# Kernel tuning notes

Measured on AMD Instinct MI355X. Metric: run time of the kernel, lower is better.

Reference implementation:

```python
import jax, jax.numpy as jnp
import numpy as np

NUM_HEADS = 8
HIDDEN_DIM = 256
QUERY_DIM = 256
HEAD_DIM = HIDDEN_DIM // NUM_HEADS
NORM_FACT = float(HIDDEN_DIM / NUM_HEADS) ** (-0.5)


def setup_inputs() -> dict:
    key = jax.random.key(0)
    k1, k2, k3, k4, k5 = jax.random.split(key, 5)
    B, Q, H, W = 16, 100, 64, 64
    q = jax.random.normal(k1, (B, Q, QUERY_DIM), dtype=jnp.float32)
    k = jax.random.normal(k2, (B, QUERY_DIM, H, W), dtype=jnp.float32)
    mask = jax.random.randint(k3, (B, H, W), 0, 2).astype(jnp.bool_)
    # xavier_uniform for [hidden, query] linear weights
    limit = float(np.sqrt(6.0 / (HIDDEN_DIM + QUERY_DIM)))
    Wq = jax.random.uniform(k4, (HIDDEN_DIM, QUERY_DIM), minval=-limit, maxval=limit, dtype=jnp.float32)
    Wk = jax.random.uniform(k5, (HIDDEN_DIM, QUERY_DIM), minval=-limit, maxval=limit, dtype=jnp.float32)
    bq = jnp.zeros((HIDDEN_DIM,), dtype=jnp.float32)
    bk = jnp.zeros((HIDDEN_DIM,), dtype=jnp.float32)
    return {"q": q, "k": k, "Wq": Wq, "bq": bq, "Wk": Wk, "bk": bk, "mask": mask}


def reference(q, k, Wq, bq, Wk, bk, mask):
    B, Q, _ = q.shape
    _, C, H, W = k.shape
    # q projection: [B, Q, hidden]
    qp = jnp.einsum('bqc,hc->bqh', q, Wq) + bq
    # k projection via 1x1 conv == channelwise linear: [B, hidden, H, W]
    kp = jnp.einsum('bchw,oc->bohw', k, Wk) + bk[None, :, None, None]
    # split heads: qh [B,Q,nh,hd], kh [B,nh,hd,H,W]
    qh = qp.reshape(B, Q, NUM_HEADS, HEAD_DIM)
    kh = kp.reshape(B, NUM_HEADS, HEAD_DIM, H, W)
    # scores [B,Q,nh,H,W]
    weights = jnp.einsum('bqnd,bndhw->bqnhw', qh, kh) * NORM_FACT
    # masked fill: mask [B,H,W] -> broadcast over (Q, heads)
    weights = jnp.where(mask[:, None, None, :, :], -jnp.inf, weights)
    # softmax jointly over (heads, H, W), as in torch flatten(2)
    flat = weights.reshape(B, Q, NUM_HEADS * H * W)
    flat = jax.nn.softmax(flat, axis=-1)
    return flat.reshape(B, Q, NUM_HEADS, H, W)
```

## Files before the change

### kernel.cpp

```cpp
#include <hip/hip_runtime.h>
#include <hip/hip_bf16.h>
#include <math.h>

#define BB 16
#define QQ 100
#define NH 8
#define HD 32
#define HWN 4096
#define NORM_FACT 0.17677669529663687f
#define QPAD 112

typedef short bf16x8_t __attribute__((ext_vector_type(8)));
typedef float f32x4_t  __attribute__((ext_vector_type(4)));

__device__ __forceinline__ unsigned short bf16bits(float f) {
    __hip_bfloat16 h = __float2bfloat16(f);
    return __builtin_bit_cast(unsigned short, h);
}
__device__ __forceinline__ float bf16tof(unsigned short u) {
    union { unsigned int i; float f; } x; x.i = (unsigned int)u << 16; return x.f;
}

__global__ void k_prep(const float* __restrict__ Wq, const float* __restrict__ Wk,
                       float* __restrict__ WqT, unsigned short* __restrict__ Wkbf) {
    int idx = blockIdx.x;
    int h = threadIdx.x;
    if (idx < 256) {
        WqT[idx * 256 + h] = Wq[h * 256 + idx];
    } else {
        int r = idx - 256;
        Wkbf[r * 256 + h] = bf16bits(Wk[r * 256 + h]);
    }
}

__global__ __launch_bounds__(256) void k_qproj(const float* __restrict__ q,
                                               const float* __restrict__ WqT,
                                               const float* __restrict__ bq,
                                               unsigned short* __restrict__ qphi,
                                               unsigned short* __restrict__ qplo) {
    int blk = blockIdx.x;
    int b = blk / 28, q0 = (blk % 28) * 4;
    int h = threadIdx.x;
    size_t obase = ((size_t)b * QPAD + q0) * 256 + h;
    if (q0 >= QQ) {
#pragma unroll
        for (int i = 0; i < 4; ++i) { qphi[obase + i * 256] = 0; qplo[obase + i * 256] = 0; }
        return;
    }
    __shared__ float qsh[4][256];
    int ibase = (b * QQ + q0) * 256;
#pragma unroll
    for (int i = 0; i < 4; ++i) qsh[i][h] = q[ibase + i * 256 + h];
    __syncthreads();
    float bias = bq[h];
    float a0 = bias, a1 = bias, a2 = bias, a3 = bias;
    for (int c = 0; c < 256; ++c) {
        float wv = WqT[c * 256 + h];
        a0 = fmaf(qsh[0][c], wv, a0);
        a1 = fmaf(qsh[1][c], wv, a1);
        a2 = fmaf(qsh[2][c], wv, a2);
        a3 = fmaf(qsh[3][c], wv, a3);
    }
    float a[4] = {a0 * NORM_FACT, a1 * NORM_FACT, a2 * NORM_FACT, a3 * NORM_FACT};
#pragma unroll
    for (int i = 0; i < 4; ++i) {
        unsigned short hi = bf16bits(a[i]);
        qphi[obase + i * 256] = hi;
        qplo[obase + i * 256] = bf16bits(a[i] - bf16tof(hi));
    }
}

__global__ __launch_bounds__(256) void k_tconv(const float* __restrict__ k,
                                               unsigned short* __restrict__ kT) {
    int b = blockIdx.z, c0 = blockIdx.y * 64, hw0 = blockIdx.x * 64;
    int t = threadIdx.x;
    __shared__ float lds[64][65];
    const float* src = k + ((size_t)b * 256 + c0) * HWN + hw0;
    int col = t & 63, r0 = t >> 6;
#pragma unroll
    for (int i = 0; i < 16; ++i) {
        int r = i * 4 + r0;
        lds[r][col] = src[(size_t)r * HWN + col];
    }
    __syncthreads();
    int hw = t >> 2, cc = (t & 3) * 16;
    unsigned short* dst = kT + ((size_t)b * HWN + hw0 + hw) * 256 + c0 + cc;
    uint4 v0, v1;
    unsigned int* w0 = (unsigned int*)&v0;
    unsigned int* w1 = (unsigned int*)&v1;
#pragma unroll
    for (int j = 0; j < 4; ++j) {
        w0[j] = (unsigned int)bf16bits(lds[cc + 2*j + 0][hw])
              | ((unsigned int)bf16bits(lds[cc + 2*j + 1][hw]) << 16);
        w1[j] = (unsigned int)bf16bits(lds[cc + 8 + 2*j + 0][hw])
              | ((unsigned int)bf16bits(lds[cc + 8 + 2*j + 1][hw]) << 16);
    }
    *(uint4*)(dst)     = v0;
    *(uint4*)(dst + 8) = v1;
}

__global__ __launch_bounds__(256) void k_kproj(const unsigned short* __restrict__ kT,
                                               const unsigned short* __restrict__ Wkbf,
                                               const float* __restrict__ bk,
                                               unsigned short* __restrict__ kpT) {
    int b = blockIdx.y;
    int hwblk = blockIdx.x * 32;
    int t = threadIdx.x;
    int w = t >> 6, lane = t & 63;
    int hwt = w & 1, oh = w >> 1;
    int n15 = lane & 15;
    int kg = lane >> 4;
    int hw = hwblk + hwt * 16 + n15;

    f32x4_t acc[8];
#pragma unroll
    for (int m = 0; m < 8; ++m) acc[m] = f32x4_t{0.f, 0.f, 0.f, 0.f};

    const unsigned short* kTrow = kT + ((size_t)b * HWN + hw) * 256 + kg * 8;
    const unsigned short* wbase = Wkbf + ((size_t)(oh * 128 + n15)) * 256 + kg * 8;

#pragma unroll 2
    for (int ks = 0; ks < 8; ++ks) {
        bf16x8_t bfrag = *reinterpret_cast<const bf16x8_t*>(kTrow + ks * 32);
#pragma unroll
        for (int m = 0; m < 8; ++m) {
            bf16x8_t afrag = *reinterpret_cast<const bf16x8_t*>(wbase + (size_t)m * 16 * 256 + ks * 32);
            acc[m] = __builtin_amdgcn_mfma_f32_16x16x32_bf16(afrag, bfrag, acc[m], 0, 0, 0);
        }
    }

    __shared__ unsigned short tile2[32 * 264];
    int hw_l = hwt * 16 + n15;
#pragma unroll
    for (int m = 0; m < 8; ++m) {
        ushort4 pk;
        unsigned short* pkp = (unsigned short*)&pk;
#pragma unroll
        for (int r = 0; r < 4; ++r) {
            int o = oh * 128 + m * 16 + kg * 4 + r;
            pkp[r] = bf16bits(acc[m][r] + bk[o]);
        }
        *(ushort4*)&tile2[hw_l * 264 + oh * 128 + m * 16 + kg * 4] = pk;
    }
    __syncthreads();
    int row = t >> 3, sub = t & 7;
    unsigned short* dst = kpT + ((size_t)b * HWN + hwblk + row) * 256 + sub * 32;
    const unsigned short* srcl = &tile2[row * 264 + sub * 32];
#pragma unroll
    for (int j = 0; j < 4; ++j)
        *(uint4*)(dst + j * 8) = *(const uint4*)(srcl + j * 8);
}

__global__ __launch_bounds__(256) void k_sums(const unsigned short* __restrict__ qphi,
                                              const unsigned short* __restrict__ qplo,
                                              const unsigned short* __restrict__ kpT,
                                              const int* __restrict__ mask,
                                              float* __restrict__ partial) {
    int b = blockIdx.y;
    int hwblk = blockIdx.x * 64;
    int t = threadIdx.x, w = t >> 6, lane = t & 63;
    int n15 = lane & 15, kg = lane >> 4;
    int hw = hwblk + w * 16 + n15;
    float mm = mask[b * HWN + hw] ? 0.0f : 1.0f;
    const unsigned short* brow  = kpT  + ((size_t)(b * HWN + hw)) * 256 + kg * 8;
    const unsigned short* ahi_b = qphi + ((size_t)(b * QPAD + n15)) * 256 + kg * 8;
    const unsigned short* alo_b = qplo + ((size_t)(b * QPAD + n15)) * 256 + kg * 8;
    float sums[7][4] = {};
#pragma unroll 1
    for (int n = 0; n < NH; ++n) {
        bf16x8_t ahi[7], alo[7];
#pragma unroll
        for (int mt = 0; mt < 7; ++mt) {
            ahi[mt] = *reinterpret_cast<const bf16x8_t*>(ahi_b + (size_t)(mt * 16) * 256 + n * 32);
            alo[mt] = *reinterpret_cast<const bf16x8_t*>(alo_b + (size_t)(mt * 16) * 256 + n * 32);
        }
        bf16x8_t bfr = *reinterpret_cast<const bf16x8_t*>(brow + n * 32);
#pragma unroll
        for (int mt = 0; mt < 7; ++mt) {
            f32x4_t a2 = {0.f, 0.f, 0.f, 0.f};
            a2 = __builtin_amdgcn_mfma_f32_16x16x32_bf16(ahi[mt], bfr, a2, 0, 0, 0);
            a2 = __builtin_amdgcn_mfma_f32_16x16x32_bf16(alo[mt], bfr, a2, 0, 0, 0);
#pragma unroll
            for (int r = 0; r < 4; ++r)
                sums[mt][r] += __expf(a2[r]) * mm;
        }
    }
#pragma unroll
    for (int mt = 0; mt < 7; ++mt)
#pragma unroll
        for (int r = 0; r < 4; ++r) {
            float v = sums[mt][r];
            v += __shfl_xor(v, 1, 64);
            v += __shfl_xor(v, 2, 64);
            v += __shfl_xor(v, 4, 64);
            v += __shfl_xor(v, 8, 64);
            if (n15 == 0) {
                int qrow = mt * 16 + kg * 4 + r;
                partial[((size_t)b * QPAD + qrow) * 256 + blockIdx.x * 4 + w] = v;
            }
        }
}

__global__ __launch_bounds__(256) void k_invsum(const float* __restrict__ partial,
                                                float* __restrict__ inv) {
    int blk = blockIdx.x;
    int b = blk / QQ, qq = blk % QQ;
    const float* p = partial + ((size_t)b * QPAD + qq) * 256;
    int t = threadIdx.x;
    float v = p[t];
#pragma unroll
    for (int off = 32; off; off >>= 1) v += __shfl_xor(v, off, 64);
    __shared__ float red[4];
    if ((t & 63) == 0) red[t >> 6] = v;
    __syncthreads();
    if (t == 0) inv[blk] = 1.0f / (red[0] + red[1] + red[2] + red[3]);
}

__global__ __launch_bounds__(256) void k_write(const unsigned short* __restrict__ qphi,
                                               const unsigned short* __restrict__ qplo,
                                               const unsigned short* __restrict__ kpT,
                                               const int* __restrict__ mask,
                                               const float* __restrict__ inv,
                                               float* __restrict__ out) {
    int hws = blockIdx.x, qt = blockIdx.y, b = blockIdx.z;
    int t = threadIdx.x, w = t >> 6, lane = t & 63;
    int n15 = lane & 15, kg = lane >> 4;
    int hw0 = hws * 256 + w * 64;
    float mm[4];
#pragma unroll
    for (int ht = 0; ht < 4; ++ht)
        mm[ht] = mask[b * HWN + hw0 + ht * 16 + n15] ? 0.0f : 1.0f;
    float invq[4];
#pragma unroll
    for (int r = 0; r < 4; ++r) {
        int qrow = qt * 16 + kg * 4 + r;
        invq[r] = (qrow < QQ) ? inv[b * QQ + qrow] : 0.0f;
    }
    const unsigned short* ahi_b = qphi + ((size_t)(b * QPAD + qt * 16 + n15)) * 256 + kg * 8;
    const unsigned short* alo_b = qplo + ((size_t)(b * QPAD + qt * 16 + n15)) * 256 + kg * 8;
    const unsigned short* brow  = kpT  + ((size_t)(b * HWN + hw0 + n15)) * 256 + kg * 8;
    __shared__ float lt[4][16][68];
#pragma unroll 1
    for (int n = 0; n < NH; ++n) {
        bf16x8_t bf[4];
#pragma unroll
        for (int ht = 0; ht < 4; ++ht)
            bf[ht] = *reinterpret_cast<const bf16x8_t*>(brow + (size_t)(ht * 16) * 256 + n * 32);
        bf16x8_t ahi = *reinterpret_cast<const bf16x8_t*>(ahi_b + n * 32);
        bf16x8_t alo = *reinterpret_cast<const bf16x8_t*>(alo_b + n * 32);
#pragma unroll
        for (int ht = 0; ht < 4; ++ht) {
            f32x4_t acc = {0.f, 0.f, 0.f, 0.f};
            acc = __builtin_amdgcn_mfma_f32_16x16x32_bf16(ahi, bf[ht], acc, 0, 0, 0);
            acc = __builtin_amdgcn_mfma_f32_16x16x32_bf16(alo, bf[ht], acc, 0, 0, 0);
#pragma unroll
            for (int r = 0; r < 4; ++r)
                lt[w][kg * 4 + r][ht * 16 + n15] = __expf(acc[r]) * mm[ht] * invq[r];
        }
#pragma unroll
        for (int j = 0; j < 4; ++j) {
            int rr = j * 4 + kg;
            int qrow = qt * 16 + rr;
            f32x4_t v4 = *(const f32x4_t*)&lt[w][rr][n15 * 4];
            if (qrow < QQ)
                __builtin_nontemporal_store(v4,
                    (f32x4_t*)(out + (((size_t)(b * QQ + qrow)) * NH + n) * HWN + hw0 + n15 * 4));
        }
    }
}

extern "C" void kernel_launch(void* const* d_in, const int* in_sizes, int n_in,
                              void* d_out, int out_size, void* d_ws, size_t ws_size,
                              hipStream_t stream) {
    const float* q    = (const float*)d_in[0];
    const float* k    = (const float*)d_in[1];
    const float* Wq   = (const float*)d_in[2];
    const float* bq   = (const float*)d_in[3];
    const float* Wk   = (const float*)d_in[4];
    const float* bk   = (const float*)d_in[5];
    const int*   mask = (const int*)d_in[6];
    float* out = (float*)d_out;

    char* base = (char*)d_ws;
    unsigned short* kT   = (unsigned short*)(base);
    unsigned short* kpT  = (unsigned short*)(base + 33554432);
    unsigned short* qphi = (unsigned short*)(base + 67108864);
    unsigned short* qplo = (unsigned short*)(base + 68026368);
    float*  WqT     = (float*)(base + 68943872);
    unsigned short* Wkbf = (unsigned short*)(base + 69206016);
    float*  partial = (float*)(base + 69337088);
    float*  inv     = (float*)(base + 71172096);
    if (ws_size < (size_t)71178496) return;

    k_prep  <<<dim3(512), dim3(256), 0, stream>>>(Wq, Wk, WqT, Wkbf);
    k_qproj <<<dim3(448), dim3(256), 0, stream>>>(q, WqT, bq, qphi, qplo);
    k_tconv <<<dim3(64, 4, 16), dim3(256), 0, stream>>>(k, kT);
    k_kproj <<<dim3(128, 16), dim3(256), 0, stream>>>(kT, Wkbf, bk, kpT);
    k_sums  <<<dim3(64, 16), dim3(256), 0, stream>>>(qphi, qplo, kpT, mask, partial);
    k_invsum<<<dim3(1600), dim3(256), 0, stream>>>(partial, inv);
    k_write <<<dim3(16, 7, 16), dim3(256), 0, stream>>>(qphi, qplo, kpT, mask, inv, out);
}
```

Before: 223.0 us.

## Fuse k transpose into projection and regrid sums and write kernels by head

Drops the separate transpose/convert kernel. k_kproj2 now loads fp32 k tiles into LDS and converts them to bf16 fragments inside the MFMA loop, which removes a 32MB intermediate round trip. k_sums now launches one block per head instead of looping over heads, so partial sums grow to 2048 slots per row and k_invsum must reduce more values. k_write is regridded by head and loops over query tiles, and it drops the LDS staging in favour of direct scalar nontemporal stores, which may give less coalesced writes.

```diff
diff --git a/kernel.cpp b/kernel.cpp
--- a/kernel.cpp
+++ b/kernel.cpp
@@ -5,10 +5,10 @@
 #define BB 16
 #define QQ 100
 #define NH 8
-#define HD 32
 #define HWN 4096
 #define NORM_FACT 0.17677669529663687f
 #define QPAD 112
+#define NSLOT 2048
 
 typedef short bf16x8_t __attribute__((ext_vector_type(8)));
 typedef float f32x4_t  __attribute__((ext_vector_type(4)));
@@ -70,67 +70,59 @@
     }
 }
 
-__global__ __launch_bounds__(256) void k_tconv(const float* __restrict__ k,
-                                               unsigned short* __restrict__ kT) {
-    int b = blockIdx.z, c0 = blockIdx.y * 64, hw0 = blockIdx.x * 64;
-    int t = threadIdx.x;
-    __shared__ float lds[64][65];
-    const float* src = k + ((size_t)b * 256 + c0) * HWN + hw0;
-    int col = t & 63, r0 = t >> 6;
-#pragma unroll
-    for (int i = 0; i < 16; ++i) {
-        int r = i * 4 + r0;
-        lds[r][col] = src[(size_t)r * HWN + col];
-    }
-    __syncthreads();
-    int hw = t >> 2, cc = (t & 3) * 16;
-    unsigned short* dst = kT + ((size_t)b * HWN + hw0 + hw) * 256 + c0 + cc;
-    uint4 v0, v1;
-    unsigned int* w0 = (unsigned int*)&v0;
-    unsigned int* w1 = (unsigned int*)&v1;
-#pragma unroll
-    for (int j = 0; j < 4; ++j) {
-        w0[j] = (unsigned int)bf16bits(lds[cc + 2*j + 0][hw])
-              | ((unsigned int)bf16bits(lds[cc + 2*j + 1][hw]) << 16);
-        w1[j] = (unsigned int)bf16bits(lds[cc + 8 + 2*j + 0][hw])
-              | ((unsigned int)bf16bits(lds[cc + 8 + 2*j + 1][hw]) << 16);
-    }
-    *(uint4*)(dst)     = v0;
-    *(uint4*)(dst + 8) = v1;
-}
-
-__global__ __launch_bounds__(256) void k_kproj(const unsigned short* __restrict__ kT,
-                                               const unsigned short* __restrict__ Wkbf,
-                                               const float* __restrict__ bk,
-                                               unsigned short* __restrict__ kpT) {
+__global__ __launch_bounds__(256) void k_kproj2(const float* __restrict__ k,
+                                                const unsigned short* __restrict__ Wkbf,
+                                                const float* __restrict__ bk,
+                                                unsigned short* __restrict__ kpT) {
     int b = blockIdx.y;
     int hwblk = blockIdx.x * 32;
     int t = threadIdx.x;
     int w = t >> 6, lane = t & 63;
     int hwt = w & 1, oh = w >> 1;
-    int n15 = lane & 15;
-    int kg = lane >> 4;
-    int hw = hwblk + hwt * 16 + n15;
+    int n15 = lane & 15, kg = lane >> 4;
+
+    __shared__ float lds_f[32][268];
+    {
+        const float* kb = k + (size_t)b * 256 * HWN + hwblk;
+        int c_l = t >> 3, l8 = t & 7;
+#pragma unroll
+        for (int it = 0; it < 8; ++it) {
+            int c = it * 32 + c_l;
+            float4 v = *(const float4*)(kb + (size_t)c * HWN + l8 * 4);
+            lds_f[l8 * 4 + 0][c] = v.x;
+            lds_f[l8 * 4 + 1][c] = v.y;
+            lds_f[l8 * 4 + 2][c] = v.z;
+            lds_f[l8 * 4 + 3][c] = v.w;
+        }
+    }
+    __syncthreads();
 
     f32x4_t acc[8];
 #pragma unroll
     for (int m = 0; m < 8; ++m) acc[m] = f32x4_t{0.f, 0.f, 0.f, 0.f};
 
-    const unsigned short* kTrow = kT + ((size_t)b * HWN + hw) * 256 + kg * 8;
     const unsigned short* wbase = Wkbf + ((size_t)(oh * 128 + n15)) * 256 + kg * 8;
-
-#pragma unroll 2
+    int hw_l = hwt * 16 + n15;
+
+#pragma unroll
     for (int ks = 0; ks < 8; ++ks) {
-        bf16x8_t bfrag = *reinterpret_cast<const bf16x8_t*>(kTrow + ks * 32);
+        f32x4_t f0 = *(const f32x4_t*)&lds_f[hw_l][ks * 32 + kg * 8];
+        f32x4_t f1 = *(const f32x4_t*)&lds_f[hw_l][ks * 32 + kg * 8 + 4];
+        bf16x8_t bfrag;
+#pragma unroll
+        for (int j = 0; j < 4; ++j) {
+            bfrag[j]     = (short)bf16bits(f0[j]);
+            bfrag[4 + j] = (short)bf16bits(f1[j]);
+        }
 #pragma unroll
         for (int m = 0; m < 8; ++m) {
             bf16x8_t afrag = *reinterpret_cast<const bf16x8_t*>(wbase + (size_t)m * 16 * 256 + ks * 32);
             acc[m] = __builtin_amdgcn_mfma_f32_16x16x32_bf16(afrag, bfrag, acc[m], 0, 0, 0);
         }
     }
-
-    __shared__ unsigned short tile2[32 * 264];
-    int hw_l = hwt * 16 + n15;
+    __syncthreads();
+
+    unsigned short* tile2 = (unsigned short*)lds_f;
 #pragma unroll
     for (int m = 0; m < 8; ++m) {
         ushort4 pk;
@@ -140,12 +132,12 @@
             int o = oh * 128 + m * 16 + kg * 4 + r;
             pkp[r] = bf16bits(acc[m][r] + bk[o]);
         }
-        *(ushort4*)&tile2[hw_l * 264 + oh * 128 + m * 16 + kg * 4] = pk;
+        *(ushort4*)&tile2[(size_t)hw_l * 264 + oh * 128 + m * 16 + kg * 4] = pk;
     }
     __syncthreads();
     int row = t >> 3, sub = t & 7;
     unsigned short* dst = kpT + ((size_t)b * HWN + hwblk + row) * 256 + sub * 32;
-    const unsigned short* srcl = &tile2[row * 264 + sub * 32];
+    const unsigned short* srcl = &tile2[(size_t)row * 264 + sub * 32];
 #pragma unroll
     for (int j = 0; j < 4; ++j)
         *(uint4*)(dst + j * 8) = *(const uint4*)(srcl + j * 8);
@@ -156,58 +148,46 @@
                                               const unsigned short* __restrict__ kpT,
                                               const int* __restrict__ mask,
                                               float* __restrict__ partial) {
-    int b = blockIdx.y;
-    int hwblk = blockIdx.x * 64;
+    int hwb = blockIdx.x, n = blockIdx.y, b = blockIdx.z;
     int t = threadIdx.x, w = t >> 6, lane = t & 63;
     int n15 = lane & 15, kg = lane >> 4;
-    int hw = hwblk + w * 16 + n15;
+    int hw = hwb * 64 + w * 16 + n15;
     float mm = mask[b * HWN + hw] ? 0.0f : 1.0f;
-    const unsigned short* brow  = kpT  + ((size_t)(b * HWN + hw)) * 256 + kg * 8;
-    const unsigned short* ahi_b = qphi + ((size_t)(b * QPAD + n15)) * 256 + kg * 8;
-    const unsigned short* alo_b = qplo + ((size_t)(b * QPAD + n15)) * 256 + kg * 8;
-    float sums[7][4] = {};
-#pragma unroll 1
-    for (int n = 0; n < NH; ++n) {
-        bf16x8_t ahi[7], alo[7];
-#pragma unroll
-        for (int mt = 0; mt < 7; ++mt) {
-            ahi[mt] = *reinterpret_cast<const bf16x8_t*>(ahi_b + (size_t)(mt * 16) * 256 + n * 32);
-            alo[mt] = *reinterpret_cast<const bf16x8_t*>(alo_b + (size_t)(mt * 16) * 256 + n * 32);
-        }
-        bf16x8_t bfr = *reinterpret_cast<const bf16x8_t*>(brow + n * 32);
-#pragma unroll
-        for (int mt = 0; mt < 7; ++mt) {
-            f32x4_t a2 = {0.f, 0.f, 0.f, 0.f};
-            a2 = __builtin_amdgcn_mfma_f32_16x16x32_bf16(ahi[mt], bfr, a2, 0, 0, 0);
-            a2 = __builtin_amdgcn_mfma_f32_16x16x32_bf16(alo[mt], bfr, a2, 0, 0, 0);
-#pragma unroll
-            for (int r = 0; r < 4; ++r)
-                sums[mt][r] += __expf(a2[r]) * mm;
-        }
-    }
-#pragma unroll
-    for (int mt = 0; mt < 7; ++mt)
+    bf16x8_t bfr = *reinterpret_cast<const bf16x8_t*>(
+        kpT + ((size_t)(b * HWN + hw)) * 256 + n * 32 + kg * 8);
+    const unsigned short* ahi_b = qphi + ((size_t)(b * QPAD + n15)) * 256 + n * 32 + kg * 8;
+    const unsigned short* alo_b = qplo + ((size_t)(b * QPAD + n15)) * 256 + n * 32 + kg * 8;
+    int slot = (hwb * 4 + w) * 8 + n;
+    float* pbase = partial + (size_t)b * QPAD * NSLOT + slot;
+#pragma unroll
+    for (int mt = 0; mt < 7; ++mt) {
+        bf16x8_t ahi = *reinterpret_cast<const bf16x8_t*>(ahi_b + (size_t)(mt * 16) * 256);
+        bf16x8_t alo = *reinterpret_cast<const bf16x8_t*>(alo_b + (size_t)(mt * 16) * 256);
+        f32x4_t a2 = {0.f, 0.f, 0.f, 0.f};
+        a2 = __builtin_amdgcn_mfma_f32_16x16x32_bf16(ahi, bfr, a2, 0, 0, 0);
+        a2 = __builtin_amdgcn_mfma_f32_16x16x32_bf16(alo, bfr, a2, 0, 0, 0);
 #pragma unroll
         for (int r = 0; r < 4; ++r) {
-            float v = sums[mt][r];
+            float v = __expf(a2[r]) * mm;
             v += __shfl_xor(v, 1, 64);
             v += __shfl_xor(v, 2, 64);
             v += __shfl_xor(v, 4, 64);
             v += __shfl_xor(v, 8, 64);
-            if (n15 == 0) {
-                int qrow = mt * 16 + kg * 4 + r;
-                partial[((size_t)b * QPAD + qrow) * 256 + blockIdx.x * 4 + w] = v;
-            }
-        }
+            if (n15 == 0)
+                pbase[(size_t)(mt * 16 + kg * 4 + r) * NSLOT] = v;
+        }
+    }
 }
 
 __global__ __launch_bounds__(256) void k_invsum(const float* __restrict__ partial,
                                                 float* __restrict__ inv) {
     int blk = blockIdx.x;
     int b = blk / QQ, qq = blk % QQ;
-    const float* p = partial + ((size_t)b * QPAD + qq) * 256;
+    const float* p = partial + ((size_t)b * QPAD + qq) * NSLOT;
     int t = threadIdx.x;
-    float v = p[t];
+    float v = 0.0f;
+#pragma unroll
+    for (int j = 0; j < NSLOT / 256; ++j) v += p[t + j * 256];
 #pragma unroll
     for (int off = 32; off; off >>= 1) v += __shfl_xor(v, off, 64);
     __shared__ float red[4];
@@ -222,7 +202,7 @@
                                                const int* __restrict__ mask,
                                                const float* __restrict__ inv,
                                                float* __restrict__ out) {
-    int hws = blockIdx.x, qt = blockIdx.y, b = blockIdx.z;
+    int hws = blockIdx.x, n = blockIdx.y, b = blockIdx.z;
     int t = threadIdx.x, w = t >> 6, lane = t & 63;
     int n15 = lane & 15, kg = lane >> 4;
     int hw0 = hws * 256 + w * 64;
@@ -230,41 +210,36 @@
 #pragma unroll
     for (int ht = 0; ht < 4; ++ht)
         mm[ht] = mask[b * HWN + hw0 + ht * 16 + n15] ? 0.0f : 1.0f;
-    float invq[4];
-#pragma unroll
-    for (int r = 0; r < 4; ++r) {
-        int qrow = qt * 16 + kg * 4 + r;
-        invq[r] = (qrow < QQ) ? inv[b * QQ + qrow] : 0.0f;
-    }
-    const unsigned short* ahi_b = qphi + ((size_t)(b * QPAD + qt * 16 + n15)) * 256 + kg * 8;
-    const unsigned short* alo_b = qplo + ((size_t)(b * QPAD + qt * 16 + n15)) * 256 + kg * 8;
-    const unsigned short* brow  = kpT  + ((size_t)(b * HWN + hw0 + n15)) * 256 + kg * 8;
-    __shared__ float lt[4][16][68];
-#pragma unroll 1
-    for (int n = 0; n < NH; ++n) {
-        bf16x8_t bf[4];
-#pragma unroll
-        for (int ht = 0; ht < 4; ++ht)
-            bf[ht] = *reinterpret_cast<const bf16x8_t*>(brow + (size_t)(ht * 16) * 256 + n * 32);
-        bf16x8_t ahi = *reinterpret_cast<const bf16x8_t*>(ahi_b + n * 32);
-        bf16x8_t alo = *reinterpret_cast<const bf16x8_t*>(alo_b + n * 32);
+    bf16x8_t bf[4];
+#pragma unroll
+    for (int ht = 0; ht < 4; ++ht)
+        bf[ht] = *reinterpret_cast<const bf16x8_t*>(
+            kpT + ((size_t)(b * HWN + hw0 + ht * 16 + n15)) * 256 + n * 32 + kg * 8);
+    const unsigned short* ahi_b = qphi + ((size_t)(b * QPAD + n15)) * 256 + n * 32 + kg * 8;
+    const unsigned short* alo_b = qplo + ((size_t)(b * QPAD + n15)) * 256 + n * 32 + kg * 8;
+#pragma unroll 2
+    for (int qt = 0; qt < 7; ++qt) {
+        bf16x8_t ahi = *reinterpret_cast<const bf16x8_t*>(ahi_b + (size_t)(qt * 16) * 256);
+        bf16x8_t alo = *reinterpret_cast<const bf16x8_t*>(alo_b + (size_t)(qt * 16) * 256);
+        float invq[4];
+#pragma unroll
+        for (int r = 0; r < 4; ++r) {
+            int qrow = qt * 16 + kg * 4 + r;
+            invq[r] = (qrow < QQ) ? inv[b * QQ + qrow] : 0.0f;
+        }
 #pragma unroll
         for (int ht = 0; ht < 4; ++ht) {
             f32x4_t acc = {0.f, 0.f, 0.f, 0.f};
             acc = __builtin_amdgcn_mfma_f32_16x16x32_bf16(ahi, bf[ht], acc, 0, 0, 0);
             acc = __builtin_amdgcn_mfma_f32_16x16x32_bf16(alo, bf[ht], acc, 0, 0, 0);
 #pragma unroll
-            for (int r = 0; r < 4; ++r)
-                lt[w][kg * 4 + r][ht * 16 + n15] = __expf(acc[r]) * mm[ht] * invq[r];
-        }
-#pragma unroll
-        for (int j = 0; j < 4; ++j) {
-            int rr = j * 4 + kg;
-            int qrow = qt * 16 + rr;
-            f32x4_t v4 = *(const f32x4_t*)&lt[w][rr][n15 * 4];
-            if (qrow < QQ)
-                __builtin_nontemporal_store(v4,
-                    (f32x4_t*)(out + (((size_t)(b * QQ + qrow)) * NH + n) * HWN + hw0 + n15 * 4));
+            for (int r = 0; r < 4; ++r) {
+                int qrow = qt * 16 + kg * 4 + r;
+                float v = __expf(acc[r]) * mm[ht] * invq[r];
+                if (qrow < QQ)
+                    __builtin_nontemporal_store(v,
+                        out + (((size_t)(b * QQ + qrow)) * NH + n) * HWN + hw0 + ht * 16 + n15);
+            }
         }
     }
 }
@@ -282,21 +257,19 @@
     float* out = (float*)d_out;
 
     char* base = (char*)d_ws;
-    unsigned short* kT   = (unsigned short*)(base);
-    unsigned short* kpT  = (unsigned short*)(base + 33554432);
-    unsigned short* qphi = (unsigned short*)(base + 67108864);
-    unsigned short* qplo = (unsigned short*)(base + 68026368);
-    float*  WqT     = (float*)(base + 68943872);
-    unsigned short* Wkbf = (unsigned short*)(base + 69206016);
-    float*  partial = (float*)(base + 69337088);
-    float*  inv     = (float*)(base + 71172096);
-    if (ws_size < (size_t)71178496) return;
+    unsigned short* kpT  = (unsigned short*)(base);
+    unsigned short* qphi = (unsigned short*)(base + 33554432);
+    unsigned short* qplo = (unsigned short*)(base + 34471936);
+    float*  WqT     = (float*)(base + 35389440);
+    unsigned short* Wkbf = (unsigned short*)(base + 35651584);
+    float*  partial = (float*)(base + 35782656);
+    float*  inv     = (float*)(base + 50462720);
+    if (ws_size < (size_t)50469120) return;
 
     k_prep  <<<dim3(512), dim3(256), 0, stream>>>(Wq, Wk, WqT, Wkbf);
     k_qproj <<<dim3(448), dim3(256), 0, stream>>>(q, WqT, bq, qphi, qplo);
-    k_tconv <<<dim3(64, 4, 16), dim3(256), 0, stream>>>(k, kT);
-    k_kproj <<<dim3(128, 16), dim3(256), 0, stream>>>(kT, Wkbf, bk, kpT);
-    k_sums  <<<dim3(64, 16), dim3(256), 0, stream>>>(qphi, qplo, kpT, mask, partial);
+    k_kproj2<<<dim3(128, 16), dim3(256), 0, stream>>>(k, Wkbf, bk, kpT);
+    k_sums  <<<dim3(64, 8, 16), dim3(256), 0, stream>>>(qphi, qplo, kpT, mask, partial);
     k_invsum<<<dim3(1600), dim3(256), 0, stream>>>(partial, inv);
-    k_write <<<dim3(16, 7, 16), dim3(256), 0, stream>>>(qphi, qplo, kpT, mask, inv, out);
-}
+    k_write <<<dim3(16, 8, 16), dim3(256), 0, stream>>>(qphi, qplo, kpT, mask, inv, out);
+}
```

Measured after the change: 233.5 us. 4.7% more time.
